# Kernel tuning notes

Hardware: AMD Instinct MI355X
Metric: run time of the kernel (lower is better)

## Reference

```python
import math
import jax, jax.numpy as jnp
import numpy as np


def _tokenformer_theta(scores):
    # L2-normalize along last dim, scale by sqrt(n), then exact GELU (torch F.gelu default)
    n = scores.shape[-1]
    l2 = jnp.maximum(jnp.linalg.norm(scores, ord=2, axis=-1, keepdims=True), 1e-8)
    scaled = scores * (math.sqrt(n) / l2)
    return jax.nn.gelu(scaled, approximate=False)


def setup_inputs() -> dict:
    key = jax.random.key(0)
    k1, k2, k3 = jax.random.split(key, 3)
    B, T, C = 4, 2048, 1024
    heads, num_tokens = 8, 1024
    key_hd, val_hd = C // heads, 1024 // heads
    x = jax.random.normal(k1, (B, T, C), dtype=jnp.float32)
    # kaiming_uniform_(a=sqrt(5)) on [heads, num_tokens, head_dim]: bound = sqrt(6/((1+5)*fan_in)) = 1/sqrt(fan_in)
    bk = 1.0 / math.sqrt(num_tokens)
    key_tokens = jax.random.uniform(k2, (heads, num_tokens, key_hd), minval=-bk, maxval=bk, dtype=jnp.float32)
    val_tokens = jax.random.uniform(k3, (heads, num_tokens, val_hd), minval=-bk, maxval=bk, dtype=jnp.float32)
    return {"x": x, "key_tokens": key_tokens, "val_tokens": val_tokens}


def reference(x, key_tokens, val_tokens):
    B, T, C = x.shape
    H, N, Dk = key_tokens.shape
    # q: [B, H, T, Dk]
    q = x.reshape(B, T, H, Dk).transpose(0, 2, 1, 3)
    # scores: [B, H, T, N]
    scores = jnp.einsum('bhtd,hnd->bhtn', q, key_tokens)
    scores = _tokenformer_theta(scores)
    # ThresHot: hard hot-mask keeping entries above the per-row mean (straight-through quantizer)
    mask = scores > jnp.mean(scores, axis=-1, keepdims=True)
    scores = jnp.where(mask, scores, 0.0)
    # out: [B, H, T, Dv] -> [B, T, H*Dv]
    out = jnp.einsum('bhtn,hnv->bhtv', scores, val_tokens)
    return out.transpose(0, 2, 1, 3).reshape(B, T, -1)
```

## Files before the change

### kernel.cpp

```cpp
#include <hip/hip_runtime.h>
#include <cstdint>
#include <cmath>


typedef __bf16 bf16x8 __attribute__((ext_vector_type(8)));
typedef float  f32x16 __attribute__((ext_vector_type(16)));
typedef float  f32x4  __attribute__((ext_vector_type(4)));
typedef unsigned short u16x8 __attribute__((ext_vector_type(8)));

__device__ __forceinline__ unsigned short bfbits(__bf16 b) {
  return __builtin_bit_cast(unsigned short, b);
}

__device__ __forceinline__ float gelu_exact(float v) {
  const float s = v * 0.70710678118654752f;
  const float a = fabsf(s);
  const float t = __builtin_amdgcn_rcpf(fmaf(0.3275911f, a, 1.0f));
  float p = fmaf(1.061405429f, t, -1.453152027f);
  p = fmaf(p, t, 1.421413741f);
  p = fmaf(p, t, -0.284496736f);
  p = fmaf(p, t, 0.254829592f);
  p *= t;
  const float e = __expf(-a * a);
  float er = fmaf(-p, e, 1.0f);
  er = copysignf(er, s);
  return 0.5f * v * (1.0f + er);
}

__global__ void prep_k(const float* __restrict__ key,
                       unsigned short* __restrict__ kh,
                       unsigned short* __restrict__ kl) {
  const int tid = blockIdx.x * 256 + threadIdx.x;
  const int h   = tid >> 14;
  const int kc  = (tid >> 10) & 15;
  const int n   = tid & 1023;
  const float* src = key + ((size_t)(h << 10) + n) * 128 + kc * 8;
  const float4 f0 = *(const float4*)src;
  const float4 f1 = *(const float4*)(src + 4);
  const float fv[8] = {f0.x, f0.y, f0.z, f0.w, f1.x, f1.y, f1.z, f1.w};
  u16x8 hv, lv;
#pragma unroll
  for (int e = 0; e < 8; ++e) {
    const __bf16 hb = (__bf16)fv[e];
    hv[e] = bfbits(hb);
    lv[e] = bfbits((__bf16)(fv[e] - (float)hb));
  }
  const size_t o = ((size_t)(h * 16 + kc) * 1024 + n) * 8;
  *(u16x8*)(kh + o) = hv;
  *(u16x8*)(kl + o) = lv;
}

__global__ void prep_v(const float* __restrict__ val,
                       unsigned short* __restrict__ vp) {
  const int tid = blockIdx.x * 256 + threadIdx.x;
  const int h   = tid >> 14;
  const int s2  = (tid >> 7) & 127;
  const int v   = tid & 127;
  const float* src = val + ((size_t)(h << 10) + s2 * 8) * 128 + v;
  u16x8 ov;
#pragma unroll
  for (int e = 0; e < 8; ++e) ov[e] = bfbits((__bf16)src[(size_t)e * 128]);
  *(u16x8*)(vp + ((size_t)(h * 128 + s2) * 128 + v) * 8) = ov;
}

#define RED1   131072
#define RED2   135168
#define SMEMSZ 139264

__global__ __launch_bounds__(1024, 4) void fused_mhk(
    const float* __restrict__ x,
    const unsigned short* __restrict__ k_hi,
    const unsigned short* __restrict__ k_lo,
    const unsigned short* __restrict__ v_pk,
    float* __restrict__ out)
{
  extern __shared__ char smem[];
  const int tid  = threadIdx.x;
  const int wave = tid >> 6;
  const int lane = tid & 63;
  const int l31  = lane & 31;
  const int hi   = lane >> 5;

  const int bid = blockIdx.x;
  const int h   = bid & 7;
  const int g8  = bid >> 3;
  const int b   = g8 & 3;
  const int tt  = g8 >> 2;
  const int t0  = tt * 64;

  {
    const float* xq = x + ((size_t)(b * 2048 + t0)) * 1024 + h * 128;
    const int r  = tid >> 4;
    const int kc = tid & 15;
    const float* sp = xq + (size_t)r * 1024 + kc * 8;
    const float4 f0 = *(const float4*)sp;
    const float4 f1 = *(const float4*)(sp + 4);
    const float fv[8] = {f0.x, f0.y, f0.z, f0.w, f1.x, f1.y, f1.z, f1.w};
    bf16x8 hv; u16x8 lv;
#pragma unroll
    for (int e = 0; e < 8; ++e) {
      const __bf16 hb = (__bf16)fv[e];
      hv[e] = hb;
      lv[e] = bfbits((__bf16)(fv[e] - (float)hb));
    }
    const int g = kc * 64 + (r ^ ((kc >> 1) & 7));
    *(bf16x8*)(smem + g * 16) = hv;
    *(u16x8*)(smem + 16384 + g * 16) = lv;
  }
  __syncthreads();

  f32x16 acc[2][2];
#pragma unroll
  for (int t = 0; t < 2; ++t)
#pragma unroll
    for (int qt = 0; qt < 2; ++qt)
#pragma unroll
      for (int i = 0; i < 16; ++i) acc[t][qt][i] = 0.f;

  {
    const unsigned short* kph = k_hi + (size_t)h * 131072;
    const unsigned short* kpl = k_lo + (size_t)h * 131072;
    const size_t kb = (size_t)hi * 8192 + (size_t)(wave * 64 + l31) * 8;
    const int hi64 = hi * 64;
#pragma unroll
    for (int s = 0; s < 8; ++s) {
      bf16x8 bqh[2], bql[2];
#pragma unroll
      for (int qt = 0; qt < 2; ++qt) {
        const int gx = (2 * s) * 64 + hi64 + ((qt * 32 + l31) ^ s);
        bqh[qt] = *(const bf16x8*)(smem + gx * 16);
        bql[qt] = *(const bf16x8*)(smem + 16384 + gx * 16);
      }
      const unsigned short* kah = kph + kb + s * 16384;
      const unsigned short* kal = kpl + kb + s * 16384;
#pragma unroll
      for (int t = 0; t < 2; ++t) {
        const bf16x8 ah = *(const bf16x8*)(kah + t * 256);
        const bf16x8 al = *(const bf16x8*)(kal + t * 256);
        acc[t][0] = __builtin_amdgcn_mfma_f32_32x32x16_bf16(ah, bqh[0], acc[t][0], 0, 0, 0);
        acc[t][1] = __builtin_amdgcn_mfma_f32_32x32x16_bf16(ah, bqh[1], acc[t][1], 0, 0, 0);
        acc[t][0] = __builtin_amdgcn_mfma_f32_32x32x16_bf16(ah, bql[0], acc[t][0], 0, 0, 0);
        acc[t][1] = __builtin_amdgcn_mfma_f32_32x32x16_bf16(ah, bql[1], acc[t][1], 0, 0, 0);
        acc[t][0] = __builtin_amdgcn_mfma_f32_32x32x16_bf16(al, bqh[0], acc[t][0], 0, 0, 0);
        acc[t][1] = __builtin_amdgcn_mfma_f32_32x32x16_bf16(al, bqh[1], acc[t][1], 0, 0, 0);
      }
    }
  }

  float* red1 = (float*)(smem + RED1);
  float* red2 = (float*)(smem + RED2);

  float ss0 = 0.f, ss1 = 0.f;
#pragma unroll
  for (int t = 0; t < 2; ++t)
#pragma unroll
    for (int i = 0; i < 16; ++i) {
      ss0 += acc[t][0][i] * acc[t][0][i];
      ss1 += acc[t][1][i] * acc[t][1][i];
    }
  ss0 += __shfl_xor(ss0, 32);
  ss1 += __shfl_xor(ss1, 32);
  if (lane < 32) {
    red1[wave * 64 + lane]      = ss0;
    red1[wave * 64 + 32 + lane] = ss1;
  }
  __syncthreads();
  float sum0 = 0.f, sum1 = 0.f;
#pragma unroll
  for (int w = 0; w < 16; ++w) {
    sum0 += red1[w * 64 + l31];
    sum1 += red1[w * 64 + 32 + l31];
  }
  const float scale0 = 32.0f / fmaxf(sqrtf(sum0), 1e-8f);
  const float scale1 = 32.0f / fmaxf(sqrtf(sum1), 1e-8f);

  float gs0 = 0.f, gs1 = 0.f;
#pragma unroll
  for (int t = 0; t < 2; ++t)
#pragma unroll
    for (int i = 0; i < 16; ++i) {
      const float g0 = gelu_exact(acc[t][0][i] * scale0);
      acc[t][0][i] = g0; gs0 += g0;
      const float g1 = gelu_exact(acc[t][1][i] * scale1);
      acc[t][1][i] = g1; gs1 += g1;
    }
  gs0 += __shfl_xor(gs0, 32);
  gs1 += __shfl_xor(gs1, 32);
  if (lane < 32) {
    red2[wave * 64 + lane]      = gs0;
    red2[wave * 64 + 32 + lane] = gs1;
  }
  __syncthreads();
  float mean0 = 0.f, mean1 = 0.f;
#pragma unroll
  for (int w = 0; w < 16; ++w) {
    mean0 += red2[w * 64 + l31];
    mean1 += red2[w * 64 + 32 + l31];
  }
  mean0 *= (1.0f / 1024.0f);
  mean1 *= (1.0f / 1024.0f);

#pragma unroll
  for (int t = 0; t < 2; ++t) {
#pragma unroll
    for (int qt = 0; qt < 2; ++qt) {
      const float mn = qt ? mean1 : mean0;
      const int q = qt * 32 + l31;
#pragma unroll
      for (int gi = 0; gi < 4; ++gi) {
        float g0 = acc[t][qt][4 * gi + 0]; g0 = (g0 > mn) ? g0 : 0.f;
        float g1 = acc[t][qt][4 * gi + 1]; g1 = (g1 > mn) ? g1 : 0.f;
        float g2 = acc[t][qt][4 * gi + 2]; g2 = (g2 > mn) ? g2 : 0.f;
        float g3 = acc[t][qt][4 * gi + 3]; g3 = (g3 > mn) ? g3 : 0.f;
        uint2 pk;
        pk.x = (unsigned)bfbits((__bf16)g0) | ((unsigned)bfbits((__bf16)g1) << 16);
        pk.y = (unsigned)bfbits((__bf16)g2) | ((unsigned)bfbits((__bf16)g3) << 16);
        const int ng = wave * 8 + t * 4 + gi;
        const int swz = (t * 4 + gi) & 7;
        *(uint2*)(smem + (ng * 64 + (q ^ swz)) * 16 + hi * 8) = pk;
      }
    }
  }
  __syncthreads();

  const int l15 = lane & 15;
  const int l4  = lane >> 4;
  const int qt2 = wave >> 3;
  const int vt  = wave & 7;

  f32x4 o0, o1;
#pragma unroll
  for (int i = 0; i < 4; ++i) { o0[i] = 0.f; o1[i] = 0.f; }

  const unsigned short* vb = v_pk + (size_t)h * 131072 + (size_t)l4 * 1024 +
                             (size_t)(vt * 16 + l15) * 8;
  const int qa = qt2 * 32 + l15;
#pragma unroll 8
  for (int ks = 0; ks < 32; ++ks) {
    const int swz = (ks & 1) * 4 + l4;
    const int ngb = (ks * 4 + l4) * 64;
    const bf16x8 a0 = *(const bf16x8*)(smem + (ngb + (qa ^ swz)) * 16);
    const bf16x8 a1 = *(const bf16x8*)(smem + (ngb + ((qa + 16) ^ swz)) * 16);
    const bf16x8 bb = *(const bf16x8*)(vb + (size_t)ks * 4096);
    o0 = __builtin_amdgcn_mfma_f32_16x16x32_bf16(a0, bb, o0, 0, 0, 0);
    o1 = __builtin_amdgcn_mfma_f32_16x16x32_bf16(a1, bb, o1, 0, 0, 0);
  }

  float* op = out + ((size_t)(b * 2048 + t0 + qt2 * 32 + l4 * 4)) * 1024 +
              h * 128 + vt * 16 + l15;
#pragma unroll
  for (int j = 0; j < 4; ++j) {
    op[(size_t)j * 1024]        = o0[j];
    op[(size_t)(16 + j) * 1024] = o1[j];
  }
}


extern "C" void kernel_launch(void* const* d_in, const int* in_sizes, int n_in,
                              void* d_out, int out_size, void* d_ws, size_t ws_size,
                              hipStream_t stream) {
  const float* x   = (const float*)d_in[0];
  const float* key = (const float*)d_in[1];
  const float* val = (const float*)d_in[2];
  float* out = (float*)d_out;

  if (ws_size < (size_t)6 * 1024 * 1024) return;

  unsigned short* k_hi = (unsigned short*)d_ws;
  unsigned short* k_lo = k_hi + 1048576;
  unsigned short* v_pk = k_lo + 1048576;

  prep_k<<<dim3(512), dim3(256), 0, stream>>>(key, k_hi, k_lo);
  prep_v<<<dim3(512), dim3(256), 0, stream>>>(val, v_pk);
  fused_mhk<<<dim3(1024), dim3(1024), SMEMSZ, stream>>>(x, k_hi, k_lo, v_pk, out);
}
```

Baseline: 113.7 us.

## Merge prep kernels, cheaper erf polynomial, 32x32 MFMA second GEMM on half the waves

Merges the two preprocessing kernels into one launch. Replaces the GELU erf approximation with a rational polynomial of the form 1-1/u^16 and folds the L2 scale into the GELU constants. Also removes the lane<32 branch in the reduction writes. The second GEMM now runs on 8 waves using 32x32x16 MFMAs instead of 16 waves with 16x16x32, which may reduce the parallelism available for that phase.

Result: no change. 113.6 us (-0.1%).

```diff
diff --git a/kernel.cpp b/kernel.cpp
--- a/kernel.cpp
+++ b/kernel.cpp
@@ -5,62 +5,66 @@
 
 typedef __bf16 bf16x8 __attribute__((ext_vector_type(8)));
 typedef float  f32x16 __attribute__((ext_vector_type(16)));
-typedef float  f32x4  __attribute__((ext_vector_type(4)));
 typedef unsigned short u16x8 __attribute__((ext_vector_type(8)));
 
 __device__ __forceinline__ unsigned short bfbits(__bf16 b) {
   return __builtin_bit_cast(unsigned short, b);
 }
 
-__device__ __forceinline__ float gelu_exact(float v) {
-  const float s = v * 0.70710678118654752f;
+__device__ __forceinline__ float gelu_s(float raw, float c707, float chalf) {
+  const float s = raw * c707;
   const float a = fabsf(s);
-  const float t = __builtin_amdgcn_rcpf(fmaf(0.3275911f, a, 1.0f));
-  float p = fmaf(1.061405429f, t, -1.453152027f);
-  p = fmaf(p, t, 1.421413741f);
-  p = fmaf(p, t, -0.284496736f);
-  p = fmaf(p, t, 0.254829592f);
-  p *= t;
-  const float e = __expf(-a * a);
-  float er = fmaf(-p, e, 1.0f);
-  er = copysignf(er, s);
-  return 0.5f * v * (1.0f + er);
-}
-
-__global__ void prep_k(const float* __restrict__ key,
-                       unsigned short* __restrict__ kh,
-                       unsigned short* __restrict__ kl) {
-  const int tid = blockIdx.x * 256 + threadIdx.x;
-  const int h   = tid >> 14;
-  const int kc  = (tid >> 10) & 15;
-  const int n   = tid & 1023;
-  const float* src = key + ((size_t)(h << 10) + n) * 128 + kc * 8;
-  const float4 f0 = *(const float4*)src;
-  const float4 f1 = *(const float4*)(src + 4);
-  const float fv[8] = {f0.x, f0.y, f0.z, f0.w, f1.x, f1.y, f1.z, f1.w};
-  u16x8 hv, lv;
-#pragma unroll
-  for (int e = 0; e < 8; ++e) {
-    const __bf16 hb = (__bf16)fv[e];
-    hv[e] = bfbits(hb);
-    lv[e] = bfbits((__bf16)(fv[e] - (float)hb));
-  }
-  const size_t o = ((size_t)(h * 16 + kc) * 1024 + n) * 8;
-  *(u16x8*)(kh + o) = hv;
-  *(u16x8*)(kl + o) = lv;
-}
-
-__global__ void prep_v(const float* __restrict__ val,
-                       unsigned short* __restrict__ vp) {
-  const int tid = blockIdx.x * 256 + threadIdx.x;
-  const int h   = tid >> 14;
-  const int s2  = (tid >> 7) & 127;
-  const int v   = tid & 127;
-  const float* src = val + ((size_t)(h << 10) + s2 * 8) * 128 + v;
-  u16x8 ov;
-#pragma unroll
-  for (int e = 0; e < 8; ++e) ov[e] = bfbits((__bf16)src[(size_t)e * 128]);
-  *(u16x8*)(vp + ((size_t)(h * 128 + s2) * 128 + v) * 8) = ov;
+  float u = fmaf(a, 4.30638e-5f, 2.765672e-4f);
+  u = fmaf(u, a, 1.520143e-4f);
+  u = fmaf(u, a, 9.2705272e-3f);
+  u = fmaf(u, a, 4.22820123e-2f);
+  u = fmaf(u, a, 7.05230784e-2f);
+  u = fmaf(u, a, 1.0f);
+  const float r  = __builtin_amdgcn_rcpf(u);
+  const float r2 = r * r;
+  const float r4 = r2 * r2;
+  const float r8 = r4 * r4;
+  const float r16 = r8 * r8;
+  const float er = copysignf(1.0f - r16, s);
+  const float hf = raw * chalf;
+  return fmaf(hf, er, hf);
+}
+
+__global__ void prep_kv(const float* __restrict__ key,
+                        const float* __restrict__ val,
+                        unsigned short* __restrict__ kh,
+                        unsigned short* __restrict__ kl,
+                        unsigned short* __restrict__ vp) {
+  const int gid = blockIdx.x * 256 + threadIdx.x;
+  if (gid < 131072) {
+    const int h  = gid >> 14;
+    const int kc = (gid >> 10) & 15;
+    const int n  = gid & 1023;
+    const float* src = key + ((size_t)(h << 10) + n) * 128 + kc * 8;
+    const float4 f0 = *(const float4*)src;
+    const float4 f1 = *(const float4*)(src + 4);
+    const float fv[8] = {f0.x, f0.y, f0.z, f0.w, f1.x, f1.y, f1.z, f1.w};
+    u16x8 hv, lv;
+#pragma unroll
+    for (int e = 0; e < 8; ++e) {
+      const __bf16 hb = (__bf16)fv[e];
+      hv[e] = bfbits(hb);
+      lv[e] = bfbits((__bf16)(fv[e] - (float)hb));
+    }
+    const size_t o = ((size_t)(h * 16 + kc) * 1024 + n) * 8;
+    *(u16x8*)(kh + o) = hv;
+    *(u16x8*)(kl + o) = lv;
+  } else {
+    const int tid = gid - 131072;
+    const int h   = tid >> 14;
+    const int s2  = (tid >> 7) & 127;
+    const int v   = tid & 127;
+    const float* src = val + ((size_t)(h << 10) + s2 * 8) * 128 + v;
+    u16x8 ov;
+#pragma unroll
+    for (int e = 0; e < 8; ++e) ov[e] = bfbits((__bf16)src[(size_t)e * 128]);
+    *(u16x8*)(vp + ((size_t)(h * 128 + s2) * 128 + v) * 8) = ov;
+  }
 }
 
 #define RED1   131072
@@ -160,10 +164,7 @@
     }
   ss0 += __shfl_xor(ss0, 32);
   ss1 += __shfl_xor(ss1, 32);
-  if (lane < 32) {
-    red1[wave * 64 + lane]      = ss0;
-    red1[wave * 64 + 32 + lane] = ss1;
-  }
+  red1[wave * 64 + lane] = hi ? ss1 : ss0;
   __syncthreads();
   float sum0 = 0.f, sum1 = 0.f;
 #pragma unroll
@@ -173,23 +174,24 @@
   }
   const float scale0 = 32.0f / fmaxf(sqrtf(sum0), 1e-8f);
   const float scale1 = 32.0f / fmaxf(sqrtf(sum1), 1e-8f);
+  const float c707_0 = scale0 * 0.70710678118654752f;
+  const float c707_1 = scale1 * 0.70710678118654752f;
+  const float chalf0 = scale0 * 0.5f;
+  const float chalf1 = scale1 * 0.5f;
 
   float gs0 = 0.f, gs1 = 0.f;
 #pragma unroll
   for (int t = 0; t < 2; ++t)
 #pragma unroll
     for (int i = 0; i < 16; ++i) {
-      const float g0 = gelu_exact(acc[t][0][i] * scale0);
+      const float g0 = gelu_s(acc[t][0][i], c707_0, chalf0);
       acc[t][0][i] = g0; gs0 += g0;
-      const float g1 = gelu_exact(acc[t][1][i] * scale1);
+      const float g1 = gelu_s(acc[t][1][i], c707_1, chalf1);
       acc[t][1][i] = g1; gs1 += g1;
     }
   gs0 += __shfl_xor(gs0, 32);
   gs1 += __shfl_xor(gs1, 32);
-  if (lane < 32) {
-    red2[wave * 64 + lane]      = gs0;
-    red2[wave * 64 + 32 + lane] = gs1;
-  }
+  red2[wave * 64 + lane] = hi ? gs1 : gs0;
   __syncthreads();
   float mean0 = 0.f, mean1 = 0.f;
 #pragma unroll
@@ -223,35 +225,31 @@
   }
   __syncthreads();
 
-  const int l15 = lane & 15;
-  const int l4  = lane >> 4;
-  const int qt2 = wave >> 3;
-  const int vt  = wave & 7;
-
-  f32x4 o0, o1;
-#pragma unroll
-  for (int i = 0; i < 4; ++i) { o0[i] = 0.f; o1[i] = 0.f; }
-
-  const unsigned short* vb = v_pk + (size_t)h * 131072 + (size_t)l4 * 1024 +
-                             (size_t)(vt * 16 + l15) * 8;
-  const int qa = qt2 * 32 + l15;
+  if (wave >= 8) return;
+  const int qt2 = wave >> 2;
+  const int vt  = wave & 3;
+  const int q   = qt2 * 32 + l31;
+
+  f32x16 o;
+#pragma unroll
+  for (int i = 0; i < 16; ++i) o[i] = 0.f;
+
+  const unsigned short* vb = v_pk + (size_t)h * 131072 + (size_t)hi * 1024 +
+                             (size_t)(vt * 32 + l31) * 8;
 #pragma unroll 8
-  for (int ks = 0; ks < 32; ++ks) {
-    const int swz = (ks & 1) * 4 + l4;
-    const int ngb = (ks * 4 + l4) * 64;
-    const bf16x8 a0 = *(const bf16x8*)(smem + (ngb + (qa ^ swz)) * 16);
-    const bf16x8 a1 = *(const bf16x8*)(smem + (ngb + ((qa + 16) ^ swz)) * 16);
-    const bf16x8 bb = *(const bf16x8*)(vb + (size_t)ks * 4096);
-    o0 = __builtin_amdgcn_mfma_f32_16x16x32_bf16(a0, bb, o0, 0, 0, 0);
-    o1 = __builtin_amdgcn_mfma_f32_16x16x32_bf16(a1, bb, o1, 0, 0, 0);
-  }
-
-  float* op = out + ((size_t)(b * 2048 + t0 + qt2 * 32 + l4 * 4)) * 1024 +
-              h * 128 + vt * 16 + l15;
-#pragma unroll
-  for (int j = 0; j < 4; ++j) {
-    op[(size_t)j * 1024]        = o0[j];
-    op[(size_t)(16 + j) * 1024] = o1[j];
+  for (int ks = 0; ks < 64; ++ks) {
+    const int ng = 2 * ks + hi;
+    const bf16x8 aa = *(const bf16x8*)(smem + (ng * 64 + (q ^ (ng & 7))) * 16);
+    const bf16x8 bb = *(const bf16x8*)(vb + (size_t)ks * 2048);
+    o = __builtin_amdgcn_mfma_f32_32x32x16_bf16(aa, bb, o, 0, 0, 0);
+  }
+
+  float* op = out + ((size_t)(b * 2048 + t0 + qt2 * 32)) * 1024 +
+              h * 128 + vt * 32 + l31;
+#pragma unroll
+  for (int r = 0; r < 16; ++r) {
+    const int qr = (r & 3) + 8 * (r >> 2) + 4 * hi;
+    op[(size_t)qr * 1024] = o[r];
   }
 }
 
@@ -270,7 +268,6 @@
   unsigned short* k_lo = k_hi + 1048576;
   unsigned short* v_pk = k_lo + 1048576;
 
-  prep_k<<<dim3(512), dim3(256), 0, stream>>>(key, k_hi, k_lo);
-  prep_v<<<dim3(512), dim3(256), 0, stream>>>(val, v_pk);
+  prep_kv<<<dim3(1024), dim3(256), 0, stream>>>(key, val, k_hi, k_lo, v_pk);
   fused_mhk<<<dim3(1024), dim3(1024), SMEMSZ, stream>>>(x, k_hi, k_lo, v_pk, out);
 }
```
